# Kernel tuning notes

Measured on AMD Instinct MI355X. Metric: run time of the kernel, lower is better.

## Reference

```python
import jax, jax.numpy as jnp
import numpy as np

HEAD_DIM = 64
NUM_Q_HEADS = 16
NUM_KV_HEADS = 4
MIN_TS = 1.0
MAX_TS = 10000.0


def _timescale(d):
    frac = 2.0 * jnp.arange(d // 2, dtype=jnp.float32) / d
    return MIN_TS * (MAX_TS / MIN_TS) ** frac  # [d/2]


def _rope(v, pos):
    # v: [B,S,H,D] float, pos: [B,S] int
    ts = _timescale(v.shape[-1])
    sinu = pos[:, :, None, None].astype(jnp.float32) / ts  # [B,S,1,D/2]
    sin, cos = jnp.sin(sinu), jnp.cos(sinu)
    x1, x2 = jnp.split(v.astype(jnp.float32), 2, axis=-1)
    return jnp.concatenate([x1 * cos - x2 * sin, x2 * cos + x1 * sin], axis=-1)


def setup_inputs() -> dict:
    key = jax.random.key(0)
    ks = jax.random.split(key, 5)
    B, S, E = 2, 2048, 1024
    Hq, Hk, D = NUM_Q_HEADS, NUM_KV_HEADS, HEAD_DIM
    sc = 0.02
    x = jax.random.normal(ks[0], (B, S, E), dtype=jnp.float32)
    q_pos = jnp.broadcast_to(jnp.arange(S, dtype=jnp.int32), (B, S))
    Wq = jax.random.normal(ks[1], (E, Hq * D), dtype=jnp.float32) * sc
    Wk = jax.random.normal(ks[2], (E, Hk * D), dtype=jnp.float32) * sc
    Wv = jax.random.normal(ks[3], (E, Hk * D), dtype=jnp.float32) * sc
    Wo = jax.random.normal(ks[4], (Hq * D, E), dtype=jnp.float32) * sc
    return {"x": x, "q_pos": q_pos, "Wq": Wq, "Wk": Wk, "Wv": Wv, "Wo": Wo}


def reference(x, q_pos, Wq, Wk, Wv, Wo):
    B, S, E = x.shape
    Hq, Hk, D = NUM_Q_HEADS, NUM_KV_HEADS, HEAD_DIM
    G = Hq // Hk  # gqa groups

    q = (x @ Wq).reshape(B, S, Hq, D)
    k = (x @ Wk).reshape(B, S, Hk, D)
    v = (x @ Wv).reshape(B, S, Hk, D)

    q = _rope(q, q_pos)  # kv_pos defaults to q_pos
    k = _rope(k, q_pos)

    # [B,Hk,G,S,D] grouped query heads vs shared kv heads
    qg = q.transpose(0, 2, 1, 3).reshape(B, Hk, G, S, D)
    kt = k.transpose(0, 2, 1, 3)  # [B,Hk,S,D]
    vt = v.transpose(0, 2, 1, 3)

    # NOTE: original uses scale=1.0 (no 1/sqrt(D))
    scores = jnp.einsum('bhgqd,bhkd->bhgqk', qg, kt)
    probs = jax.nn.softmax(scores, axis=-1)
    out = jnp.einsum('bhgqk,bhkd->bhgqd', probs, vt)  # [B,Hk,G,S,D]
    out = out.reshape(B, Hq, S, D).transpose(0, 2, 1, 3).reshape(B, S, Hq * D)
    return out @ Wo
```

## Files before the change

kernel.cpp:

```cpp
#include <hip/hip_runtime.h>
#include <hip/hip_fp16.h>
#include <math.h>

typedef __attribute__((ext_vector_type(8))) _Float16 half8;
typedef __attribute__((ext_vector_type(4))) _Float16 half4;
typedef __attribute__((ext_vector_type(4))) float f32x4;
typedef __attribute__((ext_vector_type(16))) float f32x16;
typedef __attribute__((ext_vector_type(4))) unsigned uint4v;

#define HQ 16
#define HK 4
#define DH 64
#define NB 2
#define SEQ 2048
#define EDIM 1024
#define KD 1024

__device__ __forceinline__ void gload16(const void* g, void* l) {
  __builtin_amdgcn_global_load_lds(
      (const __attribute__((address_space(1))) void*)g,
      (__attribute__((address_space(3))) void*)l, 16, 0, 0);
}

__global__ __launch_bounds__(256) void cvt_x_kernel(const float* __restrict__ x,
                                                    _Float16* __restrict__ xh, int n4) {
  int i = blockIdx.x * 256 + threadIdx.x;
  if (i >= n4) return;
  float4 v = ((const float4*)x)[i];
  half4 h;
  h[0] = (_Float16)v.x; h[1] = (_Float16)v.y; h[2] = (_Float16)v.z; h[3] = (_Float16)v.w;
  *(half4*)(xh + (size_t)i * 4) = h;
}

__global__ __launch_bounds__(256) void rope_tab_kernel(const int* __restrict__ qpos,
                                                       float2* __restrict__ tab) {
  int i = blockIdx.x * 256 + threadIdx.x;
  int row = i >> 5, d = i & 31;
  float ang = (float)qpos[row] * expf((float)d * -0.2878231366242558f);
  float sn, cs;
  sincosf(ang, &sn, &cs);
  tab[i] = make_float2(sn, cs);
}

__global__ __launch_bounds__(256) void transpose_w_kernel(const float* __restrict__ W,
                                                          _Float16* __restrict__ WT,
                                                          int N, int row_off) {
  __shared__ float t[64][65];
  int n0 = blockIdx.x * 64, k0 = blockIdx.y * 64;
  int tid = threadIdx.x;
#pragma unroll
  for (int p = 0; p < 4; ++p) {
    int idx = tid + p * 256;
    int r = idx >> 4;
    int c4 = idx & 15;
    float4 v = *(const float4*)(W + (size_t)(k0 + r) * N + n0 + c4 * 4);
    t[r][c4 * 4 + 0] = v.x; t[r][c4 * 4 + 1] = v.y;
    t[r][c4 * 4 + 2] = v.z; t[r][c4 * 4 + 3] = v.w;
  }
  __syncthreads();
#pragma unroll
  for (int p = 0; p < 4; ++p) {
    int idx = tid + p * 256;
    int n = idx >> 4;
    int k4 = idx & 15;
    half4 h;
    h[0] = (_Float16)t[k4 * 4 + 0][n]; h[1] = (_Float16)t[k4 * 4 + 1][n];
    h[2] = (_Float16)t[k4 * 4 + 2][n]; h[3] = (_Float16)t[k4 * 4 + 3][n];
    *(half4*)(WT + (size_t)(row_off + n0 + n) * KD + k0 + k4 * 4) = h;
  }
}

__global__ __launch_bounds__(256) void transpose_v_kernel(const _Float16* __restrict__ vhp,
                                                          _Float16* __restrict__ vtp) {
  __shared__ _Float16 t[64][72];
  int bh = blockIdx.y;
  int s0 = blockIdx.x * 64;
  const _Float16* src = vhp + ((size_t)bh * SEQ + s0) * DH;
  _Float16* dst = vtp + (size_t)bh * DH * SEQ + s0;
  int tid = threadIdx.x;
#pragma unroll
  for (int p = 0; p < 2; ++p) {
    int idx = tid + p * 256;
    int r = idx >> 3, c8 = idx & 7;
    half8 v = *(const half8*)(src + (size_t)r * DH + c8 * 8);
#pragma unroll
    for (int i = 0; i < 8; ++i) t[r][c8 * 8 + i] = v[i];
  }
  __syncthreads();
#pragma unroll
  for (int p = 0; p < 2; ++p) {
    int idx = tid + p * 256;
    int d = idx >> 3, c8 = idx & 7;
    half8 v;
#pragma unroll
    for (int i = 0; i < 8; ++i) v[i] = t[c8 * 8 + i][d];
    *(half8*)(dst + (size_t)d * SEQ + c8 * 8) = v;
  }
}

#define SWZ(r, kb) ((kb) ^ (((r) & 7) << 4))

__global__ __launch_bounds__(256) void gemm_qkv_rope(
    const _Float16* __restrict__ xh, const _Float16* __restrict__ WT,
    const float2* __restrict__ rtab,
    _Float16* __restrict__ qh, _Float16* __restrict__ kh, _Float16* __restrict__ vh) {
  __shared__ char As[128 * 64 * 2];
  __shared__ char Bs[128 * 64 * 2];
  int tid = threadIdx.x, lane = tid & 63, wid = tid >> 6;
  int wr = wid >> 1, wc = wid & 1;
  int bm = blockIdx.x, bn = blockIdx.y;

  const char* Ag = (const char*)(xh + (size_t)bm * 128 * KD);
  const char* Bg = (const char*)(WT + (size_t)bn * 128 * KD);

  int colS = 16 * ((lane & 7) ^ (lane >> 3));
  int rS = (lane >> 3);

  f32x4 acc[4][4] = {};

  for (int kt = 0; kt < KD / 64; ++kt) {
#pragma unroll
    for (int p = 0; p < 4; ++p) {
      int r = (wid * 4 + p) * 8 + rS;
      gload16(Ag + (size_t)r * (KD * 2) + kt * 128 + colS, As + (wid * 4 + p) * 1024);
      gload16(Bg + (size_t)r * (KD * 2) + kt * 128 + colS, Bs + (wid * 4 + p) * 1024);
    }
    __syncthreads();
#pragma unroll
    for (int kk = 0; kk < 2; ++kk) {
      int kb = kk * 64 + (lane >> 4) * 16;
      half8 af[4], bf[4];
#pragma unroll
      for (int mf = 0; mf < 4; ++mf) {
        int r = wr * 64 + mf * 16 + (lane & 15);
        af[mf] = *(const half8*)(As + r * 128 + SWZ(r, kb));
      }
#pragma unroll
      for (int nf = 0; nf < 4; ++nf) {
        int r = wc * 64 + nf * 16 + (lane & 15);
        bf[nf] = *(const half8*)(Bs + r * 128 + SWZ(r, kb));
      }
#pragma unroll
      for (int mf = 0; mf < 4; ++mf)
#pragma unroll
        for (int nf = 0; nf < 4; ++nf)
          acc[mf][nf] = __builtin_amdgcn_mfma_f32_16x16x32_f16(af[mf], bf[nf], acc[mf][nf], 0, 0, 0);
    }
    __syncthreads();
  }

  int col0 = bn * 128 + wc * 64;
  int row_base = bm * 128 + wr * 64;
#pragma unroll
  for (int mf = 0; mf < 4; ++mf) {
#pragma unroll
    for (int j = 0; j < 4; ++j) {
      int row = row_base + mf * 16 + (lane >> 4) * 4 + j;
      int b = row >> 11, s = row & (SEQ - 1);
      if (col0 < 1024) {
        int hq = col0 >> 6;
        size_t base = (((size_t)b * HQ + hq) * SEQ + s) * DH;
#pragma unroll
        for (int nf = 0; nf < 2; ++nf) {
          int d = nf * 16 + (lane & 15);
          float2 scv = rtab[row * 32 + d];
          float x1 = acc[mf][nf][j], x2 = acc[mf][nf + 2][j];
          qh[base + d]      = (_Float16)(x1 * scv.y - x2 * scv.x);
          qh[base + d + 32] = (_Float16)(x2 * scv.y + x1 * scv.x);
        }
      } else if (col0 < 1280) {
        int hk = (col0 - 1024) >> 6;
        size_t base = (((size_t)b * HK + hk) * SEQ + s) * DH;
#pragma unroll
        for (int nf = 0; nf < 2; ++nf) {
          int d = nf * 16 + (lane & 15);
          float2 scv = rtab[row * 32 + d];
          float x1 = acc[mf][nf][j], x2 = acc[mf][nf + 2][j];
          kh[base + d]      = (_Float16)(x1 * scv.y - x2 * scv.x);
          kh[base + d + 32] = (_Float16)(x2 * scv.y + x1 * scv.x);
        }
      } else {
        int hk = (col0 - 1280) >> 6;
        size_t base = (((size_t)b * HK + hk) * SEQ + s) * DH;
#pragma unroll
        for (int nf = 0; nf < 4; ++nf) {
          int d = nf * 16 + (lane & 15);
          vh[base + d] = (_Float16)acc[mf][nf][j];
        }
      }
    }
  }
}

__global__ __launch_bounds__(256) void attn_kernel(
    const _Float16* __restrict__ qh, const _Float16* __restrict__ kh,
    const _Float16* __restrict__ vt, _Float16* __restrict__ oh) {
  __shared__ char Ks[2][128 * 64 * 2];
  __shared__ char Vs[2][64 * 128 * 2];

  int tid = threadIdx.x, lane = tid & 63, wid = tid >> 6;
  int half = lane >> 5, l31 = lane & 31;
  bool lopart = (half == 0);
  int qt = blockIdx.x, bh = blockIdx.y;
  int b = bh >> 4, hq = bh & 15, hk = hq >> 2;

  const _Float16* Qg = qh + (((size_t)b * HQ + hq) * SEQ + qt * 128 + wid * 32 + l31) * DH;
  const char* Kg = (const char*)(kh + (((size_t)b * HK + hk) * SEQ) * DH);
  const char* Vtg = (const char*)(vt + (size_t)(b * HK + hk) * DH * SEQ);

  const _Float16 l2e = (_Float16)1.44269504f;
  half8 qf[4];
#pragma unroll
  for (int ks = 0; ks < 4; ++ks) {
    half8 q0 = *(const half8*)(Qg + ks * 16 + half * 8);
#pragma unroll
    for (int i = 0; i < 8; ++i) q0[i] = q0[i] * l2e;
    qf[ks] = q0;
  }

  int colK = 16 * ((lane & 7) ^ (lane >> 3));
  int rK = lane >> 3;

  f32x16 oacc[2] = {};
  float m = -3e38f, l = 0.f;

#pragma unroll
  for (int p = 0; p < 4; ++p) {
    int r = (wid * 4 + p) * 8 + rK;
    gload16(Kg + (size_t)r * 128 + colK, Ks[0] + (wid * 4 + p) * 1024);
    int d = (wid * 4 + p) * 4 + (lane >> 4);
    int colV = ((lane & 15) * 16) ^ ((d & 7) << 4);
    gload16(Vtg + (size_t)d * (SEQ * 2) + colV, Vs[0] + (wid * 4 + p) * 1024);
  }

  int cur = 0;
  for (int kt = 0; kt < SEQ / 128; ++kt) {
    if (kt + 1 < SEQ / 128) {
#pragma unroll
      for (int p = 0; p < 4; ++p) {
        int r = (wid * 4 + p) * 8 + rK;
        gload16(Kg + (size_t)((kt + 1) * 128 + r) * 128 + colK,
                Ks[cur ^ 1] + (wid * 4 + p) * 1024);
        int d = (wid * 4 + p) * 4 + (lane >> 4);
        int colV = ((lane & 15) * 16) ^ ((d & 7) << 4);
        gload16(Vtg + (size_t)d * (SEQ * 2) + (kt + 1) * 256 + colV,
                Vs[cur ^ 1] + (wid * 4 + p) * 1024);
      }
      asm volatile("s_waitcnt vmcnt(8)" ::: "memory");
    } else {
      asm volatile("s_waitcnt vmcnt(0)" ::: "memory");
    }
    __builtin_amdgcn_s_barrier();
    const char* KsB = Ks[cur];
    const char* VsB = Vs[cur];

    f32x16 sacc[4] = {};
    __builtin_amdgcn_s_setprio(1);
#pragma unroll
    for (int b4 = 0; b4 < 4; ++b4) {
      int r = b4 * 32 + l31;
#pragma unroll
      for (int ks = 0; ks < 4; ++ks) {
        half8 kf = *(const half8*)(KsB + r * 128 + SWZ(r, ks * 32 + half * 16));
        sacc[b4] = __builtin_amdgcn_mfma_f32_32x32x16_f16(kf, qf[ks], sacc[b4], 0, 0, 0);
      }
    }
    __builtin_amdgcn_s_setprio(0);

    float pm = sacc[0][0];
#pragma unroll
    for (int b4 = 0; b4 < 4; ++b4)
#pragma unroll
      for (int r = 0; r < 16; ++r)
        if (b4 || r) pm = fmaxf(pm, sacc[b4][r]);
    pm = fmaxf(pm, __shfl_xor(pm, 32, 64));
    float mnew = fmaxf(m, pm);
    float alpha = __builtin_amdgcn_exp2f(m - mnew);
    m = mnew;
    oacc[0] *= alpha;
    oacc[1] *= alpha;
    l *= alpha;
    float ps = 0.f;

#pragma unroll
    for (int b4 = 0; b4 < 4; ++b4) {
      float e[16];
#pragma unroll
      for (int r = 0; r < 16; ++r) {
        e[r] = __builtin_amdgcn_exp2f(sacc[b4][r] - m);
        ps += e[r];
      }
      unsigned W0[4], W1[4];
#pragma unroll
      for (int qd = 0; qd < 4; ++qd) {
        W0[qd] = __builtin_bit_cast(unsigned, __builtin_amdgcn_cvt_pkrtz(e[4 * qd + 0], e[4 * qd + 1]));
        W1[qd] = __builtin_bit_cast(unsigned, __builtin_amdgcn_cvt_pkrtz(e[4 * qd + 2], e[4 * qd + 3]));
      }
      half8 pf[2];
#pragma unroll
      for (int s = 0; s < 2; ++s) {
        unsigned selA = lopart ? W0[2 * s + 1] : W0[2 * s];
        unsigned crA = (unsigned)__shfl_xor((int)selA, 32, 64);
        unsigned selB = lopart ? W1[2 * s + 1] : W1[2 * s];
        unsigned crB = (unsigned)__shfl_xor((int)selB, 32, 64);
        uint4v u;
        u[0] = lopart ? W0[2 * s] : crA;
        u[1] = lopart ? W1[2 * s] : crB;
        u[2] = lopart ? crA : W0[2 * s + 1];
        u[3] = lopart ? crB : W1[2 * s + 1];
        pf[s] = __builtin_bit_cast(half8, u);
      }
      __builtin_amdgcn_s_setprio(1);
#pragma unroll
      for (int s = 0; s < 2; ++s) {
        int kvb = b4 * 64 + s * 32 + half * 16;
#pragma unroll
        for (int dblk = 0; dblk < 2; ++dblk) {
          int d = dblk * 32 + l31;
          half8 vf = *(const half8*)(VsB + d * 256 + SWZ(d, kvb));
          oacc[dblk] = __builtin_amdgcn_mfma_f32_32x32x16_f16(vf, pf[s], oacc[dblk], 0, 0, 0);
        }
      }
      __builtin_amdgcn_s_setprio(0);
    }
    ps += __shfl_xor(ps, 32, 64);
    l += ps;
    __builtin_amdgcn_s_barrier();
    cur ^= 1;
  }

  int s = qt * 128 + wid * 32 + l31;
  float invl = 1.f / l;
  size_t base = ((size_t)b * SEQ + s) * 1024 + hq * 64;
#pragma unroll
  for (int dblk = 0; dblk < 2; ++dblk) {
#pragma unroll
    for (int qd = 0; qd < 4; ++qd) {
      half4 o;
#pragma unroll
      for (int j = 0; j < 4; ++j) o[j] = (_Float16)(oacc[dblk][qd * 4 + j] * invl);
      *(half4*)(oh + base + dblk * 32 + qd * 8 + half * 4) = o;
    }
  }
}

__global__ __launch_bounds__(256) void gemm_out(
    const _Float16* __restrict__ ah, const _Float16* __restrict__ WoT,
    float* __restrict__ out) {
  __shared__ char As[128 * 64 * 2];
  __shared__ char Bs[128 * 64 * 2];
  int tid = threadIdx.x, lane = tid & 63, wid = tid >> 6;
  int wr = wid >> 1, wc = wid & 1;
  int bm = blockIdx.x, bn = blockIdx.y;
  const char* Ag = (const char*)(ah + (size_t)bm * 128 * KD);
  const char* Bg = (const char*)(WoT + (size_t)bn * 128 * KD);
  int colS = 16 * ((lane & 7) ^ (lane >> 3));
  int rS = (lane >> 3);
  f32x4 acc[4][4] = {};

  for (int kt = 0; kt < KD / 64; ++kt) {
#pragma unroll
    for (int p = 0; p < 4; ++p) {
      int r = (wid * 4 + p) * 8 + rS;
      gload16(Ag + (size_t)r * (KD * 2) + kt * 128 + colS, As + (wid * 4 + p) * 1024);
      gload16(Bg + (size_t)r * (KD * 2) + kt * 128 + colS, Bs + (wid * 4 + p) * 1024);
    }
    __syncthreads();
#pragma unroll
    for (int kk = 0; kk < 2; ++kk) {
      int kb = kk * 64 + (lane >> 4) * 16;
      half8 af[4], bf[4];
#pragma unroll
      for (int mf = 0; mf < 4; ++mf) {
        int r = wr * 64 + mf * 16 + (lane & 15);
        af[mf] = *(const half8*)(As + r * 128 + SWZ(r, kb));
      }
#pragma unroll
      for (int nf = 0; nf < 4; ++nf) {
        int r = wc * 64 + nf * 16 + (lane & 15);
        bf[nf] = *(const half8*)(Bs + r * 128 + SWZ(r, kb));
      }
#pragma unroll
      for (int mf = 0; mf < 4; ++mf)
#pragma unroll
        for (int nf = 0; nf < 4; ++nf)
          acc[mf][nf] = __builtin_amdgcn_mfma_f32_16x16x32_f16(af[mf], bf[nf], acc[mf][nf], 0, 0, 0);
    }
    __syncthreads();
  }

  int row0 = bm * 128 + wr * 64, col0 = bn * 128 + wc * 64;
#pragma unroll
  for (int mf = 0; mf < 4; ++mf)
#pragma unroll
    for (int j = 0; j < 4; ++j) {
      int row = row0 + mf * 16 + (lane >> 4) * 4 + j;
#pragma unroll
      for (int nf = 0; nf < 4; ++nf)
        out[(size_t)row * 1024 + col0 + nf * 16 + (lane & 15)] = acc[mf][nf][j];
    }
}

extern "C" void kernel_launch(void* const* d_in, const int* in_sizes, int n_in,
                              void* d_out, int out_size, void* d_ws, size_t ws_size,
                              hipStream_t stream) {
  const float* x  = (const float*)d_in[0];
  const int* qpos = (const int*)d_in[1];
  const float* Wq = (const float*)d_in[2];
  const float* Wk = (const float*)d_in[3];
  const float* Wv = (const float*)d_in[4];
  const float* Wo = (const float*)d_in[5];
  float* out = (float*)d_out;

  char* ws = (char*)d_ws;
  _Float16* xh  = (_Float16*)(ws);
  _Float16* WT  = (_Float16*)(ws + 8388608);
  _Float16* WoT = (_Float16*)(ws + 11534336);
  _Float16* qhp = (_Float16*)(ws + 13631488);
  _Float16* khp = (_Float16*)(ws + 22020096);
  _Float16* vhp = (_Float16*)(ws + 24117248);
  _Float16* ohp = (_Float16*)(ws + 26214400);
  float2*   rtab = (float2*)(ws + 34603008);
  _Float16* vtp = (_Float16*)(ws + 35651584);

  cvt_x_kernel<<<4096, 256, 0, stream>>>(x, xh, 1048576);
  rope_tab_kernel<<<512, 256, 0, stream>>>(qpos, rtab);
  transpose_w_kernel<<<dim3(16, 16), 256, 0, stream>>>(Wq, WT, 1024, 0);
  transpose_w_kernel<<<dim3(4, 16), 256, 0, stream>>>(Wk, WT, 256, 1024);
  transpose_w_kernel<<<dim3(4, 16), 256, 0, stream>>>(Wv, WT, 256, 1280);
  transpose_w_kernel<<<dim3(16, 16), 256, 0, stream>>>(Wo, WoT, 1024, 0);
  gemm_qkv_rope<<<dim3(32, 12), 256, 0, stream>>>(xh, WT, rtab, qhp, khp, vhp);
  transpose_v_kernel<<<dim3(32, 8), 256, 0, stream>>>(vhp, vtp);
  attn_kernel<<<dim3(16, 32), 256, 0, stream>>>(qhp, khp, vtp, ohp);
  gemm_out<<<dim3(32, 8), 256, 0, stream>>>(ohp, WoT, out);
}
```

Before: 128.7 us.

## Shrink attention blocks, drop double buffering, add lazy rescale and MFMA row sums

The attention kernel now runs 2-wave blocks covering 64 query rows, launched on twice as many blocks. It loads K/V tiles into a single LDS buffer with a full wait instead of double buffering. Online softmax skips the rescale unless the running max rises by more than 8 (in log2 units), the row max uses a tree reduction, and the row sum comes from an extra MFMA against a ones vector instead of a scalar accumulate plus shuffle. The goal is higher occupancy and fewer VALU ops. In exchange it loses load/compute overlap within a block and adds more K/V reloads from global memory.

Result: slower. 155.9 us (+21.2%).

```diff
diff --git a/kernel.cpp b/kernel.cpp
--- a/kernel.cpp
+++ b/kernel.cpp
@@ -20,6 +20,17 @@
   __builtin_amdgcn_global_load_lds(
       (const __attribute__((address_space(1))) void*)g,
       (__attribute__((address_space(3))) void*)l, 16, 0, 0);
+}
+
+__device__ __forceinline__ float vmax16(f32x16 v) {
+  float a = fmaxf(fmaxf(v[0], v[1]), v[2]);
+  a = fmaxf(fmaxf(a, v[3]), v[4]);
+  a = fmaxf(fmaxf(a, v[5]), v[6]);
+  a = fmaxf(fmaxf(a, v[7]), v[8]);
+  a = fmaxf(fmaxf(a, v[9]), v[10]);
+  a = fmaxf(fmaxf(a, v[11]), v[12]);
+  a = fmaxf(fmaxf(a, v[13]), v[14]);
+  return fmaxf(a, v[15]);
 }
 
 __global__ __launch_bounds__(256) void cvt_x_kernel(const float* __restrict__ x,
@@ -192,11 +203,11 @@
   }
 }
 
-__global__ __launch_bounds__(256) void attn_kernel(
+__global__ __launch_bounds__(128) void attn_kernel(
     const _Float16* __restrict__ qh, const _Float16* __restrict__ kh,
     const _Float16* __restrict__ vt, _Float16* __restrict__ oh) {
-  __shared__ char Ks[2][128 * 64 * 2];
-  __shared__ char Vs[2][64 * 128 * 2];
+  __shared__ char Ks[128 * 64 * 2];
+  __shared__ char Vs[64 * 128 * 2];
 
   int tid = threadIdx.x, lane = tid & 63, wid = tid >> 6;
   int half = lane >> 5, l31 = lane & 31;
@@ -204,7 +215,7 @@
   int qt = blockIdx.x, bh = blockIdx.y;
   int b = bh >> 4, hq = bh & 15, hk = hq >> 2;
 
-  const _Float16* Qg = qh + (((size_t)b * HQ + hq) * SEQ + qt * 128 + wid * 32 + l31) * DH;
+  const _Float16* Qg = qh + (((size_t)b * HQ + hq) * SEQ + qt * 64 + wid * 32 + l31) * DH;
   const char* Kg = (const char*)(kh + (((size_t)b * HK + hk) * SEQ) * DH);
   const char* Vtg = (const char*)(vt + (size_t)(b * HK + hk) * DH * SEQ);
 
@@ -217,42 +228,28 @@
     for (int i = 0; i < 8; ++i) q0[i] = q0[i] * l2e;
     qf[ks] = q0;
   }
+  half8 ones;
+#pragma unroll
+  for (int i = 0; i < 8; ++i) ones[i] = (_Float16)1.f;
 
   int colK = 16 * ((lane & 7) ^ (lane >> 3));
-  int rK = lane >> 3;
+  int rKl = lane >> 3;
 
   f32x16 oacc[2] = {};
   float m = -3e38f, l = 0.f;
 
-#pragma unroll
-  for (int p = 0; p < 4; ++p) {
-    int r = (wid * 4 + p) * 8 + rK;
-    gload16(Kg + (size_t)r * 128 + colK, Ks[0] + (wid * 4 + p) * 1024);
-    int d = (wid * 4 + p) * 4 + (lane >> 4);
-    int colV = ((lane & 15) * 16) ^ ((d & 7) << 4);
-    gload16(Vtg + (size_t)d * (SEQ * 2) + colV, Vs[0] + (wid * 4 + p) * 1024);
-  }
-
-  int cur = 0;
   for (int kt = 0; kt < SEQ / 128; ++kt) {
-    if (kt + 1 < SEQ / 128) {
-#pragma unroll
-      for (int p = 0; p < 4; ++p) {
-        int r = (wid * 4 + p) * 8 + rK;
-        gload16(Kg + (size_t)((kt + 1) * 128 + r) * 128 + colK,
-                Ks[cur ^ 1] + (wid * 4 + p) * 1024);
-        int d = (wid * 4 + p) * 4 + (lane >> 4);
-        int colV = ((lane & 15) * 16) ^ ((d & 7) << 4);
-        gload16(Vtg + (size_t)d * (SEQ * 2) + (kt + 1) * 256 + colV,
-                Vs[cur ^ 1] + (wid * 4 + p) * 1024);
-      }
-      asm volatile("s_waitcnt vmcnt(8)" ::: "memory");
-    } else {
-      asm volatile("s_waitcnt vmcnt(0)" ::: "memory");
-    }
+#pragma unroll
+    for (int p = 0; p < 8; ++p) {
+      int sb = wid * 8 + p;
+      int rK = sb * 8 + rKl;
+      gload16(Kg + (size_t)(kt * 128 + rK) * 128 + colK, Ks + sb * 1024);
+      int dV = sb * 4 + (lane >> 4);
+      int colV = ((lane & 15) * 16) ^ ((dV & 7) << 4);
+      gload16(Vtg + (size_t)dV * (SEQ * 2) + kt * 256 + colV, Vs + sb * 1024);
+    }
+    asm volatile("s_waitcnt vmcnt(0)" ::: "memory");
     __builtin_amdgcn_s_barrier();
-    const char* KsB = Ks[cur];
-    const char* VsB = Vs[cur];
 
     f32x16 sacc[4] = {};
     __builtin_amdgcn_s_setprio(1);
@@ -261,35 +258,30 @@
       int r = b4 * 32 + l31;
 #pragma unroll
       for (int ks = 0; ks < 4; ++ks) {
-        half8 kf = *(const half8*)(KsB + r * 128 + SWZ(r, ks * 32 + half * 16));
+        half8 kf = *(const half8*)(Ks + r * 128 + SWZ(r, ks * 32 + half * 16));
         sacc[b4] = __builtin_amdgcn_mfma_f32_32x32x16_f16(kf, qf[ks], sacc[b4], 0, 0, 0);
       }
     }
     __builtin_amdgcn_s_setprio(0);
 
-    float pm = sacc[0][0];
-#pragma unroll
-    for (int b4 = 0; b4 < 4; ++b4)
-#pragma unroll
-      for (int r = 0; r < 16; ++r)
-        if (b4 || r) pm = fmaxf(pm, sacc[b4][r]);
+    float pm = fmaxf(fmaxf(vmax16(sacc[0]), vmax16(sacc[1])),
+                     fmaxf(vmax16(sacc[2]), vmax16(sacc[3])));
     pm = fmaxf(pm, __shfl_xor(pm, 32, 64));
-    float mnew = fmaxf(m, pm);
-    float alpha = __builtin_amdgcn_exp2f(m - mnew);
-    m = mnew;
-    oacc[0] *= alpha;
-    oacc[1] *= alpha;
-    l *= alpha;
-    float ps = 0.f;
-
+    if (__any(pm > m + 8.f)) {
+      float mnew = fmaxf(m, pm);
+      float alpha = __builtin_amdgcn_exp2f(m - mnew);
+      m = mnew;
+      l *= alpha;
+      oacc[0] *= alpha;
+      oacc[1] *= alpha;
+    }
+
+    f32x16 psacc = {};
 #pragma unroll
     for (int b4 = 0; b4 < 4; ++b4) {
       float e[16];
 #pragma unroll
-      for (int r = 0; r < 16; ++r) {
-        e[r] = __builtin_amdgcn_exp2f(sacc[b4][r] - m);
-        ps += e[r];
-      }
+      for (int r = 0; r < 16; ++r) e[r] = __builtin_amdgcn_exp2f(sacc[b4][r] - m);
       unsigned W0[4], W1[4];
 #pragma unroll
       for (int qd = 0; qd < 4; ++qd) {
@@ -314,22 +306,21 @@
 #pragma unroll
       for (int s = 0; s < 2; ++s) {
         int kvb = b4 * 64 + s * 32 + half * 16;
+        psacc = __builtin_amdgcn_mfma_f32_32x32x16_f16(ones, pf[s], psacc, 0, 0, 0);
 #pragma unroll
         for (int dblk = 0; dblk < 2; ++dblk) {
           int d = dblk * 32 + l31;
-          half8 vf = *(const half8*)(VsB + d * 256 + SWZ(d, kvb));
+          half8 vf = *(const half8*)(Vs + d * 256 + SWZ(d, kvb));
           oacc[dblk] = __builtin_amdgcn_mfma_f32_32x32x16_f16(vf, pf[s], oacc[dblk], 0, 0, 0);
         }
       }
       __builtin_amdgcn_s_setprio(0);
     }
-    ps += __shfl_xor(ps, 32, 64);
-    l += ps;
+    l += psacc[0];
     __builtin_amdgcn_s_barrier();
-    cur ^= 1;
-  }
-
-  int s = qt * 128 + wid * 32 + l31;
+  }
+
+  int s = qt * 64 + wid * 32 + l31;
   float invl = 1.f / l;
   size_t base = ((size_t)b * SEQ + s) * 1024 + hq * 64;
 #pragma unroll
@@ -431,6 +422,6 @@
   transpose_w_kernel<<<dim3(16, 16), 256, 0, stream>>>(Wo, WoT, 1024, 0);
   gemm_qkv_rope<<<dim3(32, 12), 256, 0, stream>>>(xh, WT, rtab, qhp, khp, vhp);
   transpose_v_kernel<<<dim3(32, 8), 256, 0, stream>>>(vhp, vtp);
-  attn_kernel<<<dim3(16, 32), 256, 0, stream>>>(qhp, khp, vtp, ohp);
+  attn_kernel<<<dim3(32, 32), 128, 0, stream>>>(qhp, khp, vtp, ohp);
   gemm_out<<<dim3(32, 8), 256, 0, stream>>>(ohp, WoT, out);
 }
```

## Split attention KV range across two blocks and merge with combine kernel

Applied to the files above, without the earlier changes.

Splits the KV sequence in half along a new grid z dimension, so 1024 attention blocks run instead of 512. Each block writes a partial normalized output plus its running max and sum, and a new combine kernel merges the two halves. To fit more blocks per CU, LDS double buffering is dropped in favour of single buffers with a full vmcnt(0) wait, and the launch bound now requests 4 blocks. The cost is an extra kernel pass over the output, the loss of load/compute overlap, and reuse of the xh and WT workspace regions for the partial results.

New measurement: 155.7 us. 1.21x slower.

```diff
diff --git a/kernel.cpp b/kernel.cpp
--- a/kernel.cpp
+++ b/kernel.cpp
@@ -192,17 +192,19 @@
   }
 }
 
-__global__ __launch_bounds__(256) void attn_kernel(
+__global__ __launch_bounds__(256, 4) void attn_kernel(
     const _Float16* __restrict__ qh, const _Float16* __restrict__ kh,
-    const _Float16* __restrict__ vt, _Float16* __restrict__ oh) {
-  __shared__ char Ks[2][128 * 64 * 2];
-  __shared__ char Vs[2][64 * 128 * 2];
+    const _Float16* __restrict__ vt, _Float16* __restrict__ o0,
+    _Float16* __restrict__ o1, float2* __restrict__ ml) {
+  __shared__ char Ks[128 * 64 * 2];
+  __shared__ char Vs[64 * 128 * 2];
 
   int tid = threadIdx.x, lane = tid & 63, wid = tid >> 6;
   int half = lane >> 5, l31 = lane & 31;
   bool lopart = (half == 0);
-  int qt = blockIdx.x, bh = blockIdx.y;
+  int qt = blockIdx.x, bh = blockIdx.y, sp = blockIdx.z;
   int b = bh >> 4, hq = bh & 15, hk = hq >> 2;
+  int kv0 = sp * (SEQ / 2);
 
   const _Float16* Qg = qh + (((size_t)b * HQ + hq) * SEQ + qt * 128 + wid * 32 + l31) * DH;
   const char* Kg = (const char*)(kh + (((size_t)b * HK + hk) * SEQ) * DH);
@@ -219,40 +221,23 @@
   }
 
   int colK = 16 * ((lane & 7) ^ (lane >> 3));
-  int rK = lane >> 3;
+  int rKl = lane >> 3;
 
   f32x16 oacc[2] = {};
   float m = -3e38f, l = 0.f;
 
-#pragma unroll
-  for (int p = 0; p < 4; ++p) {
-    int r = (wid * 4 + p) * 8 + rK;
-    gload16(Kg + (size_t)r * 128 + colK, Ks[0] + (wid * 4 + p) * 1024);
-    int d = (wid * 4 + p) * 4 + (lane >> 4);
-    int colV = ((lane & 15) * 16) ^ ((d & 7) << 4);
-    gload16(Vtg + (size_t)d * (SEQ * 2) + colV, Vs[0] + (wid * 4 + p) * 1024);
-  }
-
-  int cur = 0;
-  for (int kt = 0; kt < SEQ / 128; ++kt) {
-    if (kt + 1 < SEQ / 128) {
-#pragma unroll
-      for (int p = 0; p < 4; ++p) {
-        int r = (wid * 4 + p) * 8 + rK;
-        gload16(Kg + (size_t)((kt + 1) * 128 + r) * 128 + colK,
-                Ks[cur ^ 1] + (wid * 4 + p) * 1024);
-        int d = (wid * 4 + p) * 4 + (lane >> 4);
-        int colV = ((lane & 15) * 16) ^ ((d & 7) << 4);
-        gload16(Vtg + (size_t)d * (SEQ * 2) + (kt + 1) * 256 + colV,
-                Vs[cur ^ 1] + (wid * 4 + p) * 1024);
-      }
-      asm volatile("s_waitcnt vmcnt(8)" ::: "memory");
-    } else {
-      asm volatile("s_waitcnt vmcnt(0)" ::: "memory");
-    }
+  for (int kt = 0; kt < SEQ / 2 / 128; ++kt) {
+#pragma unroll
+    for (int p = 0; p < 4; ++p) {
+      int sb = wid * 4 + p;
+      int r = sb * 8 + rKl;
+      gload16(Kg + (size_t)(kv0 + kt * 128 + r) * 128 + colK, Ks + sb * 1024);
+      int d = sb * 4 + (lane >> 4);
+      int colV = ((lane & 15) * 16) ^ ((d & 7) << 4);
+      gload16(Vtg + (size_t)d * (SEQ * 2) + (kv0 + kt * 128) * 2 + colV, Vs + sb * 1024);
+    }
+    asm volatile("s_waitcnt vmcnt(0)" ::: "memory");
     __builtin_amdgcn_s_barrier();
-    const char* KsB = Ks[cur];
-    const char* VsB = Vs[cur];
 
     f32x16 sacc[4] = {};
     __builtin_amdgcn_s_setprio(1);
@@ -261,7 +246,7 @@
       int r = b4 * 32 + l31;
 #pragma unroll
       for (int ks = 0; ks < 4; ++ks) {
-        half8 kf = *(const half8*)(KsB + r * 128 + SWZ(r, ks * 32 + half * 16));
+        half8 kf = *(const half8*)(Ks + r * 128 + SWZ(r, ks * 32 + half * 16));
         sacc[b4] = __builtin_amdgcn_mfma_f32_32x32x16_f16(kf, qf[ks], sacc[b4], 0, 0, 0);
       }
     }
@@ -317,7 +302,7 @@
 #pragma unroll
         for (int dblk = 0; dblk < 2; ++dblk) {
           int d = dblk * 32 + l31;
-          half8 vf = *(const half8*)(VsB + d * 256 + SWZ(d, kvb));
+          half8 vf = *(const half8*)(Vs + d * 256 + SWZ(d, kvb));
           oacc[dblk] = __builtin_amdgcn_mfma_f32_32x32x16_f16(vf, pf[s], oacc[dblk], 0, 0, 0);
         }
       }
@@ -326,11 +311,11 @@
     ps += __shfl_xor(ps, 32, 64);
     l += ps;
     __builtin_amdgcn_s_barrier();
-    cur ^= 1;
   }
 
   int s = qt * 128 + wid * 32 + l31;
   float invl = 1.f / l;
+  _Float16* op = sp ? o1 : o0;
   size_t base = ((size_t)b * SEQ + s) * 1024 + hq * 64;
 #pragma unroll
   for (int dblk = 0; dblk < 2; ++dblk) {
@@ -339,9 +324,36 @@
       half4 o;
 #pragma unroll
       for (int j = 0; j < 4; ++j) o[j] = (_Float16)(oacc[dblk][qd * 4 + j] * invl);
-      *(half4*)(oh + base + dblk * 32 + qd * 8 + half * 4) = o;
-    }
-  }
+      *(half4*)(op + base + dblk * 32 + qd * 8 + half * 4) = o;
+    }
+  }
+  if (half == 0)
+    ml[((size_t)(sp * NB + b) * HQ + hq) * SEQ + s] = make_float2(m, l);
+}
+
+__global__ __launch_bounds__(256) void combine_kernel(
+    const _Float16* __restrict__ o0, const _Float16* __restrict__ o1,
+    const float2* __restrict__ ml, _Float16* __restrict__ oh) {
+  int idx = blockIdx.x * 256 + threadIdx.x;
+  size_t h0 = (size_t)idx * 8;
+  int row = (int)(h0 >> 6);
+  int hq = row & 15;
+  int bs = row >> 4;
+  int b = bs >> 11, s = bs & (SEQ - 1);
+  float2 ml0 = ml[((size_t)(0 * NB + b) * HQ + hq) * SEQ + s];
+  float2 ml1 = ml[((size_t)(1 * NB + b) * HQ + hq) * SEQ + s];
+  float mm = fmaxf(ml0.x, ml1.x);
+  float w0 = __builtin_amdgcn_exp2f(ml0.x - mm) * ml0.y;
+  float w1 = __builtin_amdgcn_exp2f(ml1.x - mm) * ml1.y;
+  float inv = 1.f / (w0 + w1);
+  float s0 = w0 * inv, s1 = w1 * inv;
+  half8 v0 = *(const half8*)(o0 + h0);
+  half8 v1 = *(const half8*)(o1 + h0);
+  half8 o;
+#pragma unroll
+  for (int i = 0; i < 8; ++i)
+    o[i] = (_Float16)((float)v0[i] * s0 + (float)v1[i] * s1);
+  *(half8*)(oh + h0) = o;
 }
 
 __global__ __launch_bounds__(256) void gemm_out(
@@ -422,6 +434,8 @@
   _Float16* ohp = (_Float16*)(ws + 26214400);
   float2*   rtab = (float2*)(ws + 34603008);
   _Float16* vtp = (_Float16*)(ws + 35651584);
+  _Float16* op1 = (_Float16*)(ws);
+  float2*   mlb = (float2*)(ws + 8388608);
 
   cvt_x_kernel<<<4096, 256, 0, stream>>>(x, xh, 1048576);
   rope_tab_kernel<<<512, 256, 0, stream>>>(qpos, rtab);
@@ -431,6 +445,7 @@
   transpose_w_kernel<<<dim3(16, 16), 256, 0, stream>>>(Wo, WoT, 1024, 0);
   gemm_qkv_rope<<<dim3(32, 12), 256, 0, stream>>>(xh, WT, rtab, qhp, khp, vhp);
   transpose_v_kernel<<<dim3(32, 8), 256, 0, stream>>>(vhp, vtp);
-  attn_kernel<<<dim3(16, 32), 256, 0, stream>>>(qhp, khp, vtp, ohp);
+  attn_kernel<<<dim3(16, 32, 2), 256, 0, stream>>>(qhp, khp, vtp, ohp, op1, mlb);
+  combine_kernel<<<2048, 256, 0, stream>>>(ohp, op1, mlb, ohp);
   gemm_out<<<dim3(32, 8), 256, 0, stream>>>(ohp, WoT, out);
 }
```

## Merge prep kernels and halve GEMM M-tile to 64 rows

Applied to the files above, without the earlier changes.

Merges the x conversion and RoPE table kernels into one launch, and the four weight-transpose launches into a single 3D-grid launch, cutting launch count from ten to six. Both projection GEMMs switch from 128x128 to 64x128 tiles, doubling the block count so more CUs are occupied on the 256-CU device. The trade-off is less operand reuse per tile, so more global and LDS traffic for B, plus some idle blocks in the merged transpose grid for the smaller K/V weights.

Measured after the change: 109.2 us. 1.18x faster.

```diff
diff --git a/kernel.cpp b/kernel.cpp
--- a/kernel.cpp
+++ b/kernel.cpp
@@ -22,29 +22,40 @@
       (__attribute__((address_space(3))) void*)l, 16, 0, 0);
 }
 
-__global__ __launch_bounds__(256) void cvt_x_kernel(const float* __restrict__ x,
-                                                    _Float16* __restrict__ xh, int n4) {
-  int i = blockIdx.x * 256 + threadIdx.x;
-  if (i >= n4) return;
-  float4 v = ((const float4*)x)[i];
-  half4 h;
-  h[0] = (_Float16)v.x; h[1] = (_Float16)v.y; h[2] = (_Float16)v.z; h[3] = (_Float16)v.w;
-  *(half4*)(xh + (size_t)i * 4) = h;
-}
-
-__global__ __launch_bounds__(256) void rope_tab_kernel(const int* __restrict__ qpos,
-                                                       float2* __restrict__ tab) {
-  int i = blockIdx.x * 256 + threadIdx.x;
-  int row = i >> 5, d = i & 31;
-  float ang = (float)qpos[row] * expf((float)d * -0.2878231366242558f);
-  float sn, cs;
-  sincosf(ang, &sn, &cs);
-  tab[i] = make_float2(sn, cs);
-}
-
-__global__ __launch_bounds__(256) void transpose_w_kernel(const float* __restrict__ W,
-                                                          _Float16* __restrict__ WT,
-                                                          int N, int row_off) {
+__global__ __launch_bounds__(256) void prep_cvt_rope(
+    const float* __restrict__ x, _Float16* __restrict__ xh,
+    const int* __restrict__ qpos, float2* __restrict__ tab) {
+  int bx = blockIdx.x;
+  int tid = threadIdx.x;
+  if (bx < 4096) {
+    int i = bx * 256 + tid;
+    float4 v = ((const float4*)x)[i];
+    half4 h;
+    h[0] = (_Float16)v.x; h[1] = (_Float16)v.y; h[2] = (_Float16)v.z; h[3] = (_Float16)v.w;
+    *(half4*)(xh + (size_t)i * 4) = h;
+  } else {
+    int i = (bx - 4096) * 256 + tid;
+    int row = i >> 5, d = i & 31;
+    float ang = (float)qpos[row] * expf((float)d * -0.2878231366242558f);
+    float sn, cs;
+    sincosf(ang, &sn, &cs);
+    tab[i] = make_float2(sn, cs);
+  }
+}
+
+__global__ __launch_bounds__(256) void transpose_w4(
+    const float* __restrict__ Wq, const float* __restrict__ Wk,
+    const float* __restrict__ Wv, const float* __restrict__ Wo,
+    _Float16* __restrict__ WT, _Float16* __restrict__ WoT) {
+  int z = blockIdx.z;
+  const float* W;
+  _Float16* dst;
+  int N, roff;
+  if (z == 0)      { W = Wq; N = 1024; roff = 0;    dst = WT; }
+  else if (z == 1) { W = Wk; N = 256;  roff = 1024; dst = WT;  if (blockIdx.x >= 4) return; }
+  else if (z == 2) { W = Wv; N = 256;  roff = 1280; dst = WT;  if (blockIdx.x >= 4) return; }
+  else             { W = Wo; N = 1024; roff = 0;    dst = WoT; }
+
   __shared__ float t[64][65];
   int n0 = blockIdx.x * 64, k0 = blockIdx.y * 64;
   int tid = threadIdx.x;
@@ -66,7 +77,7 @@
     half4 h;
     h[0] = (_Float16)t[k4 * 4 + 0][n]; h[1] = (_Float16)t[k4 * 4 + 1][n];
     h[2] = (_Float16)t[k4 * 4 + 2][n]; h[3] = (_Float16)t[k4 * 4 + 3][n];
-    *(half4*)(WT + (size_t)(row_off + n0 + n) * KD + k0 + k4 * 4) = h;
+    *(half4*)(dst + (size_t)(roff + n0 + n) * KD + k0 + k4 * 4) = h;
   }
 }
 
@@ -104,35 +115,41 @@
     const _Float16* __restrict__ xh, const _Float16* __restrict__ WT,
     const float2* __restrict__ rtab,
     _Float16* __restrict__ qh, _Float16* __restrict__ kh, _Float16* __restrict__ vh) {
-  __shared__ char As[128 * 64 * 2];
+  __shared__ char As[64 * 64 * 2];
   __shared__ char Bs[128 * 64 * 2];
   int tid = threadIdx.x, lane = tid & 63, wid = tid >> 6;
   int wr = wid >> 1, wc = wid & 1;
   int bm = blockIdx.x, bn = blockIdx.y;
 
-  const char* Ag = (const char*)(xh + (size_t)bm * 128 * KD);
+  const char* Ag = (const char*)(xh + (size_t)bm * 64 * KD);
   const char* Bg = (const char*)(WT + (size_t)bn * 128 * KD);
 
   int colS = 16 * ((lane & 7) ^ (lane >> 3));
   int rS = (lane >> 3);
 
-  f32x4 acc[4][4] = {};
+  f32x4 acc[2][4] = {};
 
   for (int kt = 0; kt < KD / 64; ++kt) {
 #pragma unroll
+    for (int p = 0; p < 2; ++p) {
+      int sb = wid * 2 + p;
+      int r = sb * 8 + rS;
+      gload16(Ag + (size_t)r * (KD * 2) + kt * 128 + colS, As + sb * 1024);
+    }
+#pragma unroll
     for (int p = 0; p < 4; ++p) {
-      int r = (wid * 4 + p) * 8 + rS;
-      gload16(Ag + (size_t)r * (KD * 2) + kt * 128 + colS, As + (wid * 4 + p) * 1024);
-      gload16(Bg + (size_t)r * (KD * 2) + kt * 128 + colS, Bs + (wid * 4 + p) * 1024);
+      int sb = wid * 4 + p;
+      int r = sb * 8 + rS;
+      gload16(Bg + (size_t)r * (KD * 2) + kt * 128 + colS, Bs + sb * 1024);
     }
     __syncthreads();
 #pragma unroll
     for (int kk = 0; kk < 2; ++kk) {
       int kb = kk * 64 + (lane >> 4) * 16;
-      half8 af[4], bf[4];
-#pragma unroll
-      for (int mf = 0; mf < 4; ++mf) {
-        int r = wr * 64 + mf * 16 + (lane & 15);
+      half8 af[2], bf[4];
+#pragma unroll
+      for (int mf = 0; mf < 2; ++mf) {
+        int r = wr * 32 + mf * 16 + (lane & 15);
         af[mf] = *(const half8*)(As + r * 128 + SWZ(r, kb));
       }
 #pragma unroll
@@ -141,7 +158,7 @@
         bf[nf] = *(const half8*)(Bs + r * 128 + SWZ(r, kb));
       }
 #pragma unroll
-      for (int mf = 0; mf < 4; ++mf)
+      for (int mf = 0; mf < 2; ++mf)
 #pragma unroll
         for (int nf = 0; nf < 4; ++nf)
           acc[mf][nf] = __builtin_amdgcn_mfma_f32_16x16x32_f16(af[mf], bf[nf], acc[mf][nf], 0, 0, 0);
@@ -150,9 +167,9 @@
   }
 
   int col0 = bn * 128 + wc * 64;
-  int row_base = bm * 128 + wr * 64;
-#pragma unroll
-  for (int mf = 0; mf < 4; ++mf) {
+  int row_base = bm * 64 + wr * 32;
+#pragma unroll
+  for (int mf = 0; mf < 2; ++mf) {
 #pragma unroll
     for (int j = 0; j < 4; ++j) {
       int row = row_base + mf * 16 + (lane >> 4) * 4 + j;
@@ -347,32 +364,38 @@
 __global__ __launch_bounds__(256) void gemm_out(
     const _Float16* __restrict__ ah, const _Float16* __restrict__ WoT,
     float* __restrict__ out) {
-  __shared__ char As[128 * 64 * 2];
+  __shared__ char As[64 * 64 * 2];
   __shared__ char Bs[128 * 64 * 2];
   int tid = threadIdx.x, lane = tid & 63, wid = tid >> 6;
   int wr = wid >> 1, wc = wid & 1;
   int bm = blockIdx.x, bn = blockIdx.y;
-  const char* Ag = (const char*)(ah + (size_t)bm * 128 * KD);
+  const char* Ag = (const char*)(ah + (size_t)bm * 64 * KD);
   const char* Bg = (const char*)(WoT + (size_t)bn * 128 * KD);
   int colS = 16 * ((lane & 7) ^ (lane >> 3));
   int rS = (lane >> 3);
-  f32x4 acc[4][4] = {};
+  f32x4 acc[2][4] = {};
 
   for (int kt = 0; kt < KD / 64; ++kt) {
 #pragma unroll
+    for (int p = 0; p < 2; ++p) {
+      int sb = wid * 2 + p;
+      int r = sb * 8 + rS;
+      gload16(Ag + (size_t)r * (KD * 2) + kt * 128 + colS, As + sb * 1024);
+    }
+#pragma unroll
     for (int p = 0; p < 4; ++p) {
-      int r = (wid * 4 + p) * 8 + rS;
-      gload16(Ag + (size_t)r * (KD * 2) + kt * 128 + colS, As + (wid * 4 + p) * 1024);
-      gload16(Bg + (size_t)r * (KD * 2) + kt * 128 + colS, Bs + (wid * 4 + p) * 1024);
+      int sb = wid * 4 + p;
+      int r = sb * 8 + rS;
+      gload16(Bg + (size_t)r * (KD * 2) + kt * 128 + colS, Bs + sb * 1024);
     }
     __syncthreads();
 #pragma unroll
     for (int kk = 0; kk < 2; ++kk) {
       int kb = kk * 64 + (lane >> 4) * 16;
-      half8 af[4], bf[4];
-#pragma unroll
-      for (int mf = 0; mf < 4; ++mf) {
-        int r = wr * 64 + mf * 16 + (lane & 15);
+      half8 af[2], bf[4];
+#pragma unroll
+      for (int mf = 0; mf < 2; ++mf) {
+        int r = wr * 32 + mf * 16 + (lane & 15);
         af[mf] = *(const half8*)(As + r * 128 + SWZ(r, kb));
       }
 #pragma unroll
@@ -381,7 +404,7 @@
         bf[nf] = *(const half8*)(Bs + r * 128 + SWZ(r, kb));
       }
 #pragma unroll
-      for (int mf = 0; mf < 4; ++mf)
+      for (int mf = 0; mf < 2; ++mf)
 #pragma unroll
         for (int nf = 0; nf < 4; ++nf)
           acc[mf][nf] = __builtin_amdgcn_mfma_f32_16x16x32_f16(af[mf], bf[nf], acc[mf][nf], 0, 0, 0);
@@ -389,9 +412,9 @@
     __syncthreads();
   }
 
-  int row0 = bm * 128 + wr * 64, col0 = bn * 128 + wc * 64;
-#pragma unroll
-  for (int mf = 0; mf < 4; ++mf)
+  int row0 = bm * 64 + wr * 32, col0 = bn * 128 + wc * 64;
+#pragma unroll
+  for (int mf = 0; mf < 2; ++mf)
 #pragma unroll
     for (int j = 0; j < 4; ++j) {
       int row = row0 + mf * 16 + (lane >> 4) * 4 + j;
@@ -423,14 +446,10 @@
   float2*   rtab = (float2*)(ws + 34603008);
   _Float16* vtp = (_Float16*)(ws + 35651584);
 
-  cvt_x_kernel<<<4096, 256, 0, stream>>>(x, xh, 1048576);
-  rope_tab_kernel<<<512, 256, 0, stream>>>(qpos, rtab);
-  transpose_w_kernel<<<dim3(16, 16), 256, 0, stream>>>(Wq, WT, 1024, 0);
-  transpose_w_kernel<<<dim3(4, 16), 256, 0, stream>>>(Wk, WT, 256, 1024);
-  transpose_w_kernel<<<dim3(4, 16), 256, 0, stream>>>(Wv, WT, 256, 1280);
-  transpose_w_kernel<<<dim3(16, 16), 256, 0, stream>>>(Wo, WoT, 1024, 0);
-  gemm_qkv_rope<<<dim3(32, 12), 256, 0, stream>>>(xh, WT, rtab, qhp, khp, vhp);
+  prep_cvt_rope<<<4608, 256, 0, stream>>>(x, xh, qpos, rtab);
+  transpose_w4<<<dim3(16, 16, 4), 256, 0, stream>>>(Wq, Wk, Wv, Wo, WT, WoT);
+  gemm_qkv_rope<<<dim3(64, 12), 256, 0, stream>>>(xh, WT, rtab, qhp, khp, vhp);
   transpose_v_kernel<<<dim3(32, 8), 256, 0, stream>>>(vhp, vtp);
   attn_kernel<<<dim3(16, 32), 256, 0, stream>>>(qhp, khp, vtp, ohp);
-  gemm_out<<<dim3(32, 8), 256, 0, stream>>>(ohp, WoT, out);
-}
+  gemm_out<<<dim3(64, 8), 256, 0, stream>>>(ohp, WoT, out);
+}
```
